# Kernel optimization log

Hardware: AMD Instinct MI355X
Metric: run time of the kernel (lower is better)

## Reference

```python
import math
import jax, jax.numpy as jnp
import numpy as np

B, S, D, H = 4, 2048, 1024, 16
HD = D // H
SAMPLING_FACTOR = 5.0


def setup_inputs() -> dict:
    key = jax.random.key(0)
    ks = jax.random.split(key, 6)
    std = 1.0 / math.sqrt(D)
    inp = {
        "x": jax.random.normal(ks[0], (B, S, D), dtype=jnp.float32),
        "Wq": jax.random.normal(ks[1], (D, D), dtype=jnp.float32) * std,
        "bq": jnp.zeros((D,), dtype=jnp.float32),
        "Wk": jax.random.normal(ks[2], (D, D), dtype=jnp.float32) * std,
        "bk": jnp.zeros((D,), dtype=jnp.float32),
        "Wv": jax.random.normal(ks[3], (D, D), dtype=jnp.float32) * std,
        "bv": jnp.zeros((D,), dtype=jnp.float32),
        "Wo": jax.random.normal(ks[4], (D, D), dtype=jnp.float32) * std,
        "bo": jnp.zeros((D,), dtype=jnp.float32),
        "sample_idx": jax.random.randint(ks[5], (S,), 0, S, dtype=jnp.int32),
    }
    return inp


def reference(x, Wq, bq, Wk, bk, Wv, bv, Wo, bo, sample_idx):
    batch, seq_len, d_model = x.shape
    scale = math.sqrt(HD)
    # u = number of top (active) queries; U_part = seq_len here (sampling saturates)
    u = max(1, min(seq_len, int(SAMPLING_FACTOR * math.log(seq_len + 1))))

    def proj(W, b):
        # [B,S,D] -> [B,H,S,hd]
        return (x @ W + b).reshape(batch, seq_len, H, HD).transpose(0, 2, 1, 3)

    Q = proj(Wq, bq)
    K = proj(Wk, bk)
    V = proj(Wv, bv)

    # sparsity measure over sampled keys (with replacement)
    K_sample = K[:, :, sample_idx, :]                     # [B,H,U,hd]
    scores_sample = jnp.einsum("bhsd,bhud->bhsu", Q, K_sample) / scale
    M = scores_sample.max(axis=-1) - scores_sample.mean(axis=-1)  # [B,H,S]

    _, top_idx = jax.lax.top_k(M, u)                      # [B,H,u]

    Q_reduce = jnp.take_along_axis(Q, top_idx[..., None], axis=2)  # [B,H,u,hd]
    attn_scores = jnp.einsum("bhud,bhsd->bhus", Q_reduce, K) / scale
    attn_probs = jax.nn.softmax(attn_scores, axis=-1)
    context = jnp.einsum("bhus,bhsd->bhud", attn_probs, V)        # [B,H,u,hd]

    # fill lazy queries with mean of V, scatter active-query contexts
    V_mean = V.mean(axis=2, keepdims=True)                # [B,H,1,hd]
    out = jnp.broadcast_to(V_mean, (batch, H, seq_len, HD))
    b_idx = jnp.arange(batch)[:, None, None]
    h_idx = jnp.arange(H)[None, :, None]
    out = out.at[b_idx, h_idx, top_idx].set(context)      # [B,H,S,hd]

    out = out.transpose(0, 2, 1, 3).reshape(batch, seq_len, d_model)
    return out @ Wo + bo
```

## Files before the change

### kernel.cpp

```cpp
#include <hip/hip_runtime.h>
#include <math.h>
#include <stdint.h>
#include <stddef.h>

#define BB 4
#define SS 2048
#define DD 1024
#define HH 16
#define HD 64
#define UU 38
#define BH (BB*HH)
#define NROWS (BB*SS)
#define QSZ (BB*HH*SS*HD)
#define NSPLIT 8
#define SPLEN (SS/NSPLIT)
#define QPAD 40

typedef unsigned short ushortT;
typedef unsigned int u32;
typedef __attribute__((ext_vector_type(8))) short bf16x8;
typedef __attribute__((ext_vector_type(4))) float f32x4;

static __device__ __forceinline__ ushortT f2bf(float f) {
  union { float f; unsigned int u; } v; v.f = f;
  unsigned int r = v.u + 0x7fffu + ((v.u >> 16) & 1u);
  return (ushortT)(r >> 16);
}
static __device__ __forceinline__ float bf2f(ushortT h) {
  union { unsigned int u; float f; } v; v.u = ((unsigned int)h) << 16; return v.f;
}
static __device__ __forceinline__ void gld16(const void* g, void* l) {
  __builtin_amdgcn_global_load_lds((const __attribute__((address_space(1))) u32*)g,
                                   (__attribute__((address_space(3))) u32*)l, 16, 0, 0);
}

__global__ __launch_bounds__(256) void split_x(
    const float* __restrict__ x, ushortT* __restrict__ xh, ushortT* __restrict__ xl)
{
  size_t i = ((size_t)blockIdx.x * 256 + threadIdx.x) * 8;
  float4 v0 = *(const float4*)&x[i];
  float4 v1 = *(const float4*)&x[i + 4];
  float fv[8] = {v0.x, v0.y, v0.z, v0.w, v1.x, v1.y, v1.z, v1.w};
  bf16x8 hv, lv;
#pragma unroll
  for (int j = 0; j < 8; ++j) {
    ushortT h = f2bf(fv[j]);
    hv[j] = (short)h;
    lv[j] = (short)f2bf(fv[j] - bf2f(h));
  }
  *(bf16x8*)&xh[i] = hv;
  *(bf16x8*)&xl[i] = lv;
}

__global__ __launch_bounds__(256) void splitT_kernel(
    const float* __restrict__ W, ushortT* __restrict__ WhT, ushortT* __restrict__ WlT)
{
  __shared__ float tile[64][65];
  const int t = threadIdx.x;
  const int bk = blockIdx.y * 64, bn = blockIdx.x * 64;
  const int rr = t >> 4, c4 = (t & 15) * 4;
#pragma unroll
  for (int p = 0; p < 4; ++p) {
    int row = rr + p * 16;
    float4 v = *(const float4*)&W[(size_t)(bk + row) * DD + bn + c4];
    tile[row][c4] = v.x; tile[row][c4+1] = v.y; tile[row][c4+2] = v.z; tile[row][c4+3] = v.w;
  }
  __syncthreads();
  const int n = t & 63, ks = (t >> 6) * 16;
  union { ushortT us[16]; uint4 q[2]; } hb, lb;
#pragma unroll
  for (int j = 0; j < 16; ++j) {
    float f = tile[ks + j][n];
    ushortT h = f2bf(f);
    hb.us[j] = h;
    lb.us[j] = f2bf(f - bf2f(h));
  }
  size_t o = ((size_t)(bn + n) * DD + (size_t)(bk + ks)) >> 3;
  ((uint4*)WhT)[o] = hb.q[0]; ((uint4*)WhT)[o + 1] = hb.q[1];
  ((uint4*)WlT)[o] = lb.q[0]; ((uint4*)WlT)[o + 1] = lb.q[1];
}

__global__ __launch_bounds__(256) void dedupe_kernel(
    const int* __restrict__ sidx, int* __restrict__ uidx, int* __restrict__ ucount)
{
  __shared__ unsigned bm[64];
  __shared__ int base[64];
  const int t = threadIdx.x;
  if (t < 64) bm[t] = 0;
  __syncthreads();
  for (int s = t; s < SS; s += 256) {
    int v = sidx[s];
    atomicOr(&bm[v >> 5], 1u << (v & 31));
  }
  __syncthreads();
  if (t < 64) {
    int c = __popc(bm[t]);
    int pre = c;
#pragma unroll
    for (int off = 1; off < 64; off <<= 1) {
      int o = __shfl_up(pre, off, 64);
      if (t >= off) pre += o;
    }
    base[t] = pre - c;
    if (t == 63) ucount[0] = pre;
  }
  __syncthreads();
  if (t < 64) {
    unsigned m = bm[t];
    int o = base[t];
    while (m) {
      int b = __ffs(m) - 1;
      uidx[o++] = t * 32 + b;
      m &= m - 1;
    }
  }
  __syncthreads();
  int total = ucount[0];
  int padded = (total + 127) & ~127;
  int first = uidx[0];
  for (int i = total + t; i < padded; i += 256) uidx[i] = first;
}

__global__ __launch_bounds__(256, 4) void gemm_qkv(
    const ushortT* __restrict__ Axh, const ushortT* __restrict__ Axl,
    const ushortT* __restrict__ WqhT, const ushortT* __restrict__ WqlT,
    const ushortT* __restrict__ WkhT, const ushortT* __restrict__ WklT,
    const ushortT* __restrict__ WvhT, const ushortT* __restrict__ WvlT,
    const float* __restrict__ bq, const float* __restrict__ bk, const float* __restrict__ bv,
    ushortT* __restrict__ Qhg, ushortT* __restrict__ Qlg,
    ushortT* __restrict__ Khg, ushortT* __restrict__ Klg,
    float* __restrict__ V)
{
  __shared__ ushortT As[128 * 64];
  __shared__ ushortT Bs[128 * 64];
  const int t = threadIdx.x;
  const int lin = blockIdx.x;
  const int xcd = lin & 7;
  const int idx = lin >> 3;
  const int m_loc = idx & 7;
  const int n_idx = idx >> 3;
  const int m0 = (xcd * 8 + m_loc) * 128;
  const int p = n_idx >> 3;
  const int n0 = (n_idx & 7) * 128;
  const ushortT* Bh = (p == 0) ? WqhT : (p == 1) ? WkhT : WvhT;
  const ushortT* Bl = (p == 0) ? WqlT : (p == 1) ? WklT : WvlT;
  const float* bias = (p == 0) ? bq : (p == 1) ? bk : bv;
  const int lane = t & 63, w = t >> 6;
  const int wr = w >> 1, wc = w & 1;
  const int fr = lane & 15, fs = lane >> 4;
  const int srow = t >> 3, sslot = t & 7;
  f32x4 acc[4][4];
#pragma unroll
  for (int i = 0; i < 4; ++i)
#pragma unroll
    for (int j = 0; j < 4; ++j) acc[i][j] = (f32x4){0.f, 0.f, 0.f, 0.f};

  for (int kt = 0; kt < 48; ++kt) {
    const int seg = kt >> 4;
    const int rk0 = (kt & 15) * 64;
    const ushortT* a_src = (seg == 1) ? Axl : Axh;
    const ushortT* b_src = (seg == 2) ? Bl : Bh;
    __syncthreads();
#pragma unroll
    for (int is = 0; is < 4; ++is) {
      int row = is * 32 + srow;
      int soff = ((sslot ^ (row & 7)) * 8);
      int cb = (is * 256 + (t & 192)) * 8;
      gld16(&a_src[(size_t)(m0 + row) * DD + rk0 + soff], &As[cb]);
      gld16(&b_src[(size_t)(n0 + row) * DD + rk0 + soff], &Bs[cb]);
    }
    __syncthreads();
#pragma unroll
    for (int kk = 0; kk < 2; ++kk) {
      bf16x8 af[4], bf[4];
#pragma unroll
      for (int i = 0; i < 4; ++i) {
        int row = wr * 64 + i * 16 + fr;
        af[i] = *(const bf16x8*)&As[row * 64 + (((kk * 4 + fs) ^ (row & 7)) * 8)];
      }
#pragma unroll
      for (int j = 0; j < 4; ++j) {
        int row = wc * 64 + j * 16 + fr;
        bf[j] = *(const bf16x8*)&Bs[row * 64 + (((kk * 4 + fs) ^ (row & 7)) * 8)];
      }
#pragma unroll
      for (int i = 0; i < 4; ++i)
#pragma unroll
        for (int j = 0; j < 4; ++j)
          acc[i][j] = __builtin_amdgcn_mfma_f32_16x16x32_bf16(af[i], bf[j], acc[i][j], 0, 0, 0);
    }
  }
#pragma unroll
  for (int i = 0; i < 4; ++i) {
#pragma unroll
    for (int j = 0; j < 4; ++j) {
      int c = n0 + wc * 64 + j * 16 + fr;
      float bs = bias[c];
      int h = c >> 6, hd = c & 63;
#pragma unroll
      for (int r = 0; r < 4; ++r) {
        int m = m0 + wr * 64 + i * 16 + fs * 4 + r;
        int b = m >> 11, s = m & (SS - 1);
        size_t oidx = (((size_t)(b * HH + h)) * SS + s) * HD + hd;
        float val = acc[i][j][r] + bs;
        if (p == 2) {
          V[oidx] = val;
        } else {
          ushortT hv = f2bf(val);
          ushortT lv = f2bf(val - bf2f(hv));
          if (p == 0) { Qhg[oidx] = hv; Qlg[oidx] = lv; }
          else        { Khg[oidx] = hv; Klg[oidx] = lv; }
        }
      }
    }
  }
}

__global__ __launch_bounds__(256) void means_kernel(
    const ushortT* __restrict__ Khg, const ushortT* __restrict__ Klg,
    const float* __restrict__ V, const int* __restrict__ sidx,
    float* __restrict__ Kmean, float* __restrict__ Vmean)
{
  __shared__ float rk[4][64], rv[4][64];
  const int bh = blockIdx.x;
  const int t = threadIdx.x;
  const int d = t & 63, p = t >> 6;
  const float* Vb = V + (size_t)bh * SS * HD;
  float ka = 0.f, va = 0.f;
  for (int r = p * 512; r < (p + 1) * 512; ++r) {
    size_t ki = ((size_t)bh * SS + sidx[r]) * HD + d;
    ka += bf2f(Khg[ki]) + bf2f(Klg[ki]);
    va += Vb[(size_t)r * HD + d];
  }
  rk[p][d] = ka; rv[p][d] = va;
  __syncthreads();
  if (t < 64) {
    Kmean[bh * HD + t] = (rk[0][t] + rk[1][t] + rk[2][t] + rk[3][t]) * (1.0f / SS);
    Vmean[bh * HD + t] = (rv[0][t] + rv[1][t] + rv[2][t] + rv[3][t]) * (1.0f / SS);
  }
}

__global__ __launch_bounds__(256, 2) void m_mfma(
    const ushortT* __restrict__ Qhg, const ushortT* __restrict__ Qlg,
    const ushortT* __restrict__ Khg, const ushortT* __restrict__ Klg,
    const int* __restrict__ uidx, const int* __restrict__ ucount,
    const float* __restrict__ Kmean, float* __restrict__ M)
{
  __shared__ ushortT QhL[128 * 64], QlL[128 * 64], KhL[128 * 64], KlL[128 * 64];
  __shared__ float Mred[2][128];
  __shared__ float km[64];
  const int t = threadIdx.x;
  const int lin = blockIdx.x;
  const int swz = (lin & 7) * 128 + (lin >> 3);
  const int bh = swz >> 4;
  const int s0 = (swz & 15) * 128;
  const int lane = t & 63, w = t >> 6;
  const int wr = w >> 1, wc = w & 1;
  const int fr = lane & 15, fs = lane >> 4;
  if (t < 64) km[t] = Kmean[bh * HD + t];
  const int srow = t >> 3, sslot = t & 7;
  const int ntiles = (ucount[0] + 127) >> 7;
#pragma unroll
  for (int is = 0; is < 4; ++is) {
    int row = is * 32 + srow;
    int soff = ((sslot ^ (row & 7)) * 8);
    int cb = (is * 256 + (t & 192)) * 8;
    size_t ga = ((size_t)bh * SS + s0 + row) * HD + soff;
    gld16(&Qhg[ga], &QhL[cb]);
    gld16(&Qlg[ga], &QlL[cb]);
  }
  float runmax[4][4];
#pragma unroll
  for (int i = 0; i < 4; ++i)
#pragma unroll
    for (int r = 0; r < 4; ++r) runmax[i][r] = -INFINITY;

  for (int ui = 0; ui < ntiles; ++ui) {
    __syncthreads();
#pragma unroll
    for (int is = 0; is < 4; ++is) {
      int row = is * 32 + srow;
      int gr = uidx[ui * 128 + row];
      int soff = ((sslot ^ (row & 7)) * 8);
      int cb = (is * 256 + (t & 192)) * 8;
      size_t ga = ((size_t)bh * SS + gr) * HD + soff;
      gld16(&Khg[ga], &KhL[cb]);
      gld16(&Klg[ga], &KlL[cb]);
    }
    __syncthreads();
    f32x4 acc[4][4];
#pragma unroll
    for (int i = 0; i < 4; ++i)
#pragma unroll
      for (int j = 0; j < 4; ++j) acc[i][j] = (f32x4){0.f, 0.f, 0.f, 0.f};
#pragma unroll
    for (int kk = 0; kk < 2; ++kk) {
      bf16x8 ah[4], al[4], bh[4], bl[4];
#pragma unroll
      for (int i = 0; i < 4; ++i) {
        int row = wr * 64 + i * 16 + fr;
        int off = row * 64 + (((kk * 4 + fs) ^ (row & 7)) * 8);
        ah[i] = *(const bf16x8*)&QhL[off];
        al[i] = *(const bf16x8*)&QlL[off];
      }
#pragma unroll
      for (int j = 0; j < 4; ++j) {
        int row = wc * 64 + j * 16 + fr;
        int off = row * 64 + (((kk * 4 + fs) ^ (row & 7)) * 8);
        bh[j] = *(const bf16x8*)&KhL[off];
        bl[j] = *(const bf16x8*)&KlL[off];
      }
#pragma unroll
      for (int i = 0; i < 4; ++i)
#pragma unroll
        for (int j = 0; j < 4; ++j) {
          acc[i][j] = __builtin_amdgcn_mfma_f32_16x16x32_bf16(ah[i], bh[j], acc[i][j], 0, 0, 0);
          acc[i][j] = __builtin_amdgcn_mfma_f32_16x16x32_bf16(ah[i], bl[j], acc[i][j], 0, 0, 0);
          acc[i][j] = __builtin_amdgcn_mfma_f32_16x16x32_bf16(al[i], bh[j], acc[i][j], 0, 0, 0);
        }
    }
#pragma unroll
    for (int i = 0; i < 4; ++i)
#pragma unroll
      for (int j = 0; j < 4; ++j)
#pragma unroll
        for (int r = 0; r < 4; ++r) runmax[i][r] = fmaxf(runmax[i][r], acc[i][j][r]);
  }
#pragma unroll
  for (int i = 0; i < 4; ++i)
#pragma unroll
    for (int r = 0; r < 4; ++r) {
      float v = runmax[i][r];
      v = fmaxf(v, __shfl_xor(v, 1, 64));
      v = fmaxf(v, __shfl_xor(v, 2, 64));
      v = fmaxf(v, __shfl_xor(v, 4, 64));
      v = fmaxf(v, __shfl_xor(v, 8, 64));
      runmax[i][r] = v;
    }
  if (fr == 0) {
#pragma unroll
    for (int i = 0; i < 4; ++i)
#pragma unroll
      for (int r = 0; r < 4; ++r)
        Mred[wc][wr * 64 + i * 16 + fs * 4 + r] = runmax[i][r];
  }
  __syncthreads();
  if (t < 128) {
    float mx = fmaxf(Mred[0][t], Mred[1][t]);
    float md = 0.f;
    const ushortT* qh = &Qhg[((size_t)bh * SS + s0 + t) * HD];
    const ushortT* ql = &Qlg[((size_t)bh * SS + s0 + t) * HD];
#pragma unroll
    for (int k8 = 0; k8 < 8; ++k8) {
      bf16x8 hv = *(const bf16x8*)&qh[k8 * 8];
      bf16x8 lv = *(const bf16x8*)&ql[k8 * 8];
#pragma unroll
      for (int j = 0; j < 8; ++j)
        md += (bf2f((ushortT)hv[j]) + bf2f((ushortT)lv[j])) * km[k8 * 8 + j];
    }
    M[(size_t)bh * SS + s0 + t] = (mx - md) * 0.125f;
  }
}

__global__ __launch_bounds__(256) void topk_kernel(const float* __restrict__ M,
                                                   int* __restrict__ topi)
{
  __shared__ float rw[4];
  __shared__ int   ri4[4];
  __shared__ int   winner;
  const int t = threadIdx.x, bh = blockIdx.x;
  const int lane = t & 63, w = t >> 6;
  float v[8];
#pragma unroll
  for (int j = 0; j < 8; ++j) v[j] = M[(size_t)bh * SS + t + j * 256];
  for (int it = 0; it < UU; ++it) {
    float bv = v[0]; int bj = 0;
#pragma unroll
    for (int j = 1; j < 8; ++j) if (v[j] > bv) { bv = v[j]; bj = j; }
    int bs = t + bj * 256;
#pragma unroll
    for (int off = 32; off > 0; off >>= 1) {
      float ov = __shfl_xor(bv, off, 64);
      int os = __shfl_xor(bs, off, 64);
      if (ov > bv || (ov == bv && os < bs)) { bv = ov; bs = os; }
    }
    if (lane == 0) { rw[w] = bv; ri4[w] = bs; }
    __syncthreads();
    if (t == 0) {
      float fv = rw[0]; int fsx = ri4[0];
#pragma unroll
      for (int g = 1; g < 4; ++g)
        if (rw[g] > fv || (rw[g] == fv && ri4[g] < fsx)) { fv = rw[g]; fsx = ri4[g]; }
      topi[bh * UU + it] = fsx;
      winner = fsx;
    }
    __syncthreads();
    int wi = winner;
    if ((wi & 255) == t) {
      int jj = wi >> 8;
#pragma unroll
      for (int j = 0; j < 8; ++j) if (j == jj) v[j] = -INFINITY;
    }
  }
}

__global__ __launch_bounds__(256) void attn_flash(
    const ushortT* __restrict__ Qhg, const ushortT* __restrict__ Qlg,
    const ushortT* __restrict__ Khg, const ushortT* __restrict__ Klg,
    const float* __restrict__ V, const int* __restrict__ topi,
    float* __restrict__ pacc, float* __restrict__ pm, float* __restrict__ pl)
{
  __shared__ float Qt[64][68];
  __shared__ float KV[64][68];
  __shared__ float Ps[64][68];
  __shared__ float redA[16][64];
  __shared__ float redB[16][64];
  __shared__ float mrow[64], lrow[64], scl[64];
  const int t  = threadIdx.x;
  const int bh = blockIdx.x;
  const int sp = blockIdx.y;
  const float* Vb = V + (size_t)bh * SS * HD;
  if (t < 64) { mrow[t] = -INFINITY; lrow[t] = 0.f; }
  {
    int q = t >> 2, k4 = (t & 3) * 16;
    float fv[16];
#pragma unroll
    for (int e = 0; e < 16; ++e) fv[e] = 0.f;
    if (q < UU) {
      int qidx = topi[bh * UU + q];
      size_t ga = ((size_t)bh * SS + qidx) * HD + k4;
      bf16x8 h0 = *(const bf16x8*)&Qhg[ga];
      bf16x8 h1 = *(const bf16x8*)&Qhg[ga + 8];
      bf16x8 l0 = *(const bf16x8*)&Qlg[ga];
      bf16x8 l1 = *(const bf16x8*)&Qlg[ga + 8];
#pragma unroll
      for (int j = 0; j < 8; ++j) {
        fv[j]     = bf2f((ushortT)h0[j]) + bf2f((ushortT)l0[j]);
        fv[8 + j] = bf2f((ushortT)h1[j]) + bf2f((ushortT)l1[j]);
      }
    }
#pragma unroll
    for (int e = 0; e < 16; ++e) Qt[k4 + e][q] = fv[e];
  }
  const int q4 = (t & 15) * 4, j4g = (t >> 4) * 4, d4 = (t >> 4) * 4;
  const int lj = t >> 2, lk4 = (t & 3) * 16;
  float acc[4][4] = {};
  for (int s0 = sp * SPLEN; s0 < (sp + 1) * SPLEN; s0 += 64) {
    __syncthreads();
    {
      size_t ga = ((size_t)bh * SS + s0 + lj) * HD + lk4;
      bf16x8 h0 = *(const bf16x8*)&Khg[ga];
      bf16x8 h1 = *(const bf16x8*)&Khg[ga + 8];
      bf16x8 l0 = *(const bf16x8*)&Klg[ga];
      bf16x8 l1 = *(const bf16x8*)&Klg[ga + 8];
#pragma unroll
      for (int j = 0; j < 8; ++j) {
        KV[lk4 + j][lj]     = bf2f((ushortT)h0[j]) + bf2f((ushortT)l0[j]);
        KV[lk4 + 8 + j][lj] = bf2f((ushortT)h1[j]) + bf2f((ushortT)l1[j]);
      }
    }
    __syncthreads();
    float sacc[4][4] = {};
#pragma unroll 16
    for (int k = 0; k < 64; ++k) {
      float4 a = *(const float4*)&Qt[k][q4];
      float4 b = *(const float4*)&KV[k][j4g];
      sacc[0][0] += a.x*b.x; sacc[0][1] += a.x*b.y; sacc[0][2] += a.x*b.z; sacc[0][3] += a.x*b.w;
      sacc[1][0] += a.y*b.x; sacc[1][1] += a.y*b.y; sacc[1][2] += a.y*b.z; sacc[1][3] += a.y*b.w;
      sacc[2][0] += a.z*b.x; sacc[2][1] += a.z*b.y; sacc[2][2] += a.z*b.z; sacc[2][3] += a.z*b.w;
      sacc[3][0] += a.w*b.x; sacc[3][1] += a.w*b.y; sacc[3][2] += a.w*b.z; sacc[3][3] += a.w*b.w;
    }
#pragma unroll
    for (int i = 0; i < 4; ++i) {
      float mx = fmaxf(fmaxf(sacc[i][0], sacc[i][1]), fmaxf(sacc[i][2], sacc[i][3]));
      redA[t >> 4][q4 + i] = mx;
    }
    __syncthreads();
    if (t < 64) {
      float mx = redA[0][t];
#pragma unroll
      for (int g = 1; g < 16; ++g) mx = fmaxf(mx, redA[g][t]);
      float mn = fmaxf(mrow[t], mx * 0.125f);
      scl[t] = __expf(mrow[t] - mn);
      mrow[t] = mn;
    }
    __syncthreads();
    float4 vld[4];
#pragma unroll
    for (int i = 0; i < 4; ++i)
      vld[i] = *(const float4*)&Vb[(size_t)(s0 + lj) * HD + lk4 + 4 * i];
    float psum[4] = {};
#pragma unroll
    for (int i = 0; i < 4; ++i) {
#pragma unroll
      for (int j = 0; j < 4; ++j) {
        float e = __expf(sacc[i][j] * 0.125f - mrow[q4 + i]);
        Ps[j4g + j][q4 + i] = e;
        psum[i] += e;
      }
      redB[t >> 4][q4 + i] = psum[i];
    }
#pragma unroll
    for (int i = 0; i < 4; ++i)
      *(float4*)&KV[lj][lk4 + 4 * i] = vld[i];
    __syncthreads();
    if (t < 64) {
      float ts = redB[0][t];
#pragma unroll
      for (int g = 1; g < 16; ++g) ts += redB[g][t];
      lrow[t] = lrow[t] * scl[t] + ts;
    }
#pragma unroll
    for (int i = 0; i < 4; ++i) {
      float fsc = scl[q4 + i];
      acc[i][0] *= fsc; acc[i][1] *= fsc; acc[i][2] *= fsc; acc[i][3] *= fsc;
    }
#pragma unroll 16
    for (int j = 0; j < 64; ++j) {
      float4 a = *(const float4*)&Ps[j][q4];
      float4 b = *(const float4*)&KV[j][d4];
      acc[0][0] += a.x*b.x; acc[0][1] += a.x*b.y; acc[0][2] += a.x*b.z; acc[0][3] += a.x*b.w;
      acc[1][0] += a.y*b.x; acc[1][1] += a.y*b.y; acc[1][2] += a.y*b.z; acc[1][3] += a.y*b.w;
      acc[2][0] += a.z*b.x; acc[2][1] += a.z*b.y; acc[2][2] += a.z*b.z; acc[2][3] += a.z*b.w;
      acc[3][0] += a.w*b.x; acc[3][1] += a.w*b.y; acc[3][2] += a.w*b.z; acc[3][3] += a.w*b.w;
    }
  }
  const size_t pb = ((size_t)bh * NSPLIT + sp) * QPAD;
#pragma unroll
  for (int i = 0; i < 4; ++i) {
    int q = q4 + i;
    if (q < UU) {
#pragma unroll
      for (int j = 0; j < 4; ++j)
        pacc[(pb + q) * HD + d4 + j] = acc[i][j];
    }
  }
  if (t < UU) { pm[pb + t] = mrow[t]; pl[pb + t] = lrow[t]; }
}

__global__ __launch_bounds__(256) void attn_combine(
    const float* __restrict__ pacc, const float* __restrict__ pm,
    const float* __restrict__ pl, float* __restrict__ ctx)
{
  const int t  = threadIdx.x;
  const int bh = blockIdx.x;
  const int d = t & 63, qg = t >> 6;
  for (int q = qg; q < UU; q += 4) {
    float mv[NSPLIT];
    float ms = -INFINITY;
#pragma unroll
    for (int sp = 0; sp < NSPLIT; ++sp) {
      mv[sp] = pm[((size_t)bh * NSPLIT + sp) * QPAD + q];
      ms = fmaxf(ms, mv[sp]);
    }
    float l = 0.f, c = 0.f;
#pragma unroll
    for (int sp = 0; sp < NSPLIT; ++sp) {
      float wv = __expf(mv[sp] - ms);
      l += wv * pl[((size_t)bh * NSPLIT + sp) * QPAD + q];
      c += wv * pacc[(((size_t)bh * NSPLIT + sp) * QPAD + q) * HD + d];
    }
    ctx[((size_t)bh * UU + q) * HD + d] = c / l;
  }
}

__global__ __launch_bounds__(256) void base_kernel(
    const float* __restrict__ Vmean, const float* __restrict__ Wo,
    const float* __restrict__ bo, float* __restrict__ base)
{
  __shared__ float red[16][BB][16];
  const int t = threadIdx.x;
  const int cl = t & 15, kg = t >> 4;
  const int c = blockIdx.x * 16 + cl;
  float acc[BB] = {};
  for (int k = kg * 64; k < kg * 64 + 64; ++k) {
    float w = Wo[(size_t)k * DD + c];
#pragma unroll
    for (int b = 0; b < BB; ++b) acc[b] += Vmean[b * DD + k] * w;
  }
#pragma unroll
  for (int b = 0; b < BB; ++b) red[kg][b][cl] = acc[b];
  __syncthreads();
  if (t < 64) {
    int b = t >> 4, cc = blockIdx.x * 16 + (t & 15);
    float s = 0.f;
#pragma unroll
    for (int g = 0; g < 16; ++g) s += red[g][b][t & 15];
    base[b * DD + cc] = s + bo[cc];
  }
}

__global__ void fill_kernel(const float* __restrict__ base, float* __restrict__ out)
{
  size_t i = (size_t)blockIdx.x * 256 + threadIdx.x;
  float4 bv = ((const float4*)base)[(i >> 19) * 256 + (i & 255)];
  ((float4*)out)[i] = bv;
}

__global__ __launch_bounds__(256) void scatter_kernel(
    const float* __restrict__ ctx, const float* __restrict__ Vmean,
    const int* __restrict__ topi, const float* __restrict__ Wo,
    float* __restrict__ out)
{
  __shared__ float delta[64];
  const int t  = threadIdx.x;
  const int bh = blockIdx.x;
  const int u  = blockIdx.y;
  const int b = bh >> 4, h = bh & 15;
  const int s = topi[bh * UU + u];
  if (t < 64) delta[t] = ctx[((size_t)bh * UU + u) * HD + t] - Vmean[bh * HD + t];
  __syncthreads();
  float* orow = out + ((size_t)b * SS + s) * DD;
#pragma unroll
  for (int j = 0; j < 4; ++j) {
    int c = t + j * 256;
    float acc = 0.f;
#pragma unroll 8
    for (int d = 0; d < 64; ++d) acc += delta[d] * Wo[(size_t)(h * HD + d) * DD + c];
    atomicAdd(&orow[c], acc);
  }
}

extern "C" void kernel_launch(void* const* d_in, const int* in_sizes, int n_in,
                              void* d_out, int out_size, void* d_ws, size_t ws_size,
                              hipStream_t stream) {
  const float* x  = (const float*)d_in[0];
  const float* Wq = (const float*)d_in[1];
  const float* bq = (const float*)d_in[2];
  const float* Wk = (const float*)d_in[3];
  const float* bk = (const float*)d_in[4];
  const float* Wv = (const float*)d_in[5];
  const float* bv = (const float*)d_in[6];
  const float* Wo = (const float*)d_in[7];
  const float* bo = (const float*)d_in[8];
  const int* sidx = (const int*)d_in[9];
  float* out = (float*)d_out;

  float* f     = (float*)d_ws;
  float* V     = f;
  float* Kmean = f + (size_t)QSZ;
  float* Vmean = Kmean + BH * HD;
  float* Mbuf  = Vmean + BH * HD;
  float* base  = Mbuf + (size_t)BH * SS;
  float* ctx   = base + BB * DD;
  float* pacc  = ctx + (size_t)BH * UU * HD;
  float* pm    = pacc + (size_t)BH * NSPLIT * QPAD * HD;
  float* pl    = pm + (size_t)BH * NSPLIT * QPAD;
  int*   topi  = (int*)(pl + (size_t)BH * NSPLIT * QPAD);
  int*   uidx  = topi + 4096;
  int*   ucount= uidx + 4096;
  ushortT* usp = (ushortT*)(ucount + 64);
  ushortT* WqhT = usp;
  ushortT* WqlT = WqhT + (size_t)DD * DD;
  ushortT* WkhT = WqlT + (size_t)DD * DD;
  ushortT* WklT = WkhT + (size_t)DD * DD;
  ushortT* WvhT = WklT + (size_t)DD * DD;
  ushortT* WvlT = WvhT + (size_t)DD * DD;
  ushortT* xh   = WvlT + (size_t)DD * DD;
  ushortT* xl   = xh + (size_t)NROWS * DD;
  ushortT* Qhg  = xl + (size_t)NROWS * DD;
  ushortT* Qlg  = Qhg + (size_t)QSZ;
  ushortT* Khg  = Qlg + (size_t)QSZ;
  ushortT* Klg  = Khg + (size_t)QSZ;

  split_x<<<NROWS * DD / (256 * 8), 256, 0, stream>>>(x, xh, xl);
  dim3 gs(16, 16);
  splitT_kernel<<<gs, 256, 0, stream>>>(Wq, WqhT, WqlT);
  splitT_kernel<<<gs, 256, 0, stream>>>(Wk, WkhT, WklT);
  splitT_kernel<<<gs, 256, 0, stream>>>(Wv, WvhT, WvlT);
  dedupe_kernel<<<1, 256, 0, stream>>>(sidx, uidx, ucount);
  gemm_qkv<<<1536, 256, 0, stream>>>(xh, xl, WqhT, WqlT, WkhT, WklT, WvhT, WvlT,
                                     bq, bk, bv, Qhg, Qlg, Khg, Klg, V);
  means_kernel<<<BH, 256, 0, stream>>>(Khg, Klg, V, sidx, Kmean, Vmean);
  m_mfma<<<1024, 256, 0, stream>>>(Qhg, Qlg, Khg, Klg, uidx, ucount, Kmean, Mbuf);
  topk_kernel<<<BH, 256, 0, stream>>>(Mbuf, topi);
  attn_flash<<<dim3(BH, NSPLIT), 256, 0, stream>>>(Qhg, Qlg, Khg, Klg, V, topi, pacc, pm, pl);
  attn_combine<<<BH, 256, 0, stream>>>(pacc, pm, pl, ctx);
  base_kernel<<<DD / 16, 256, 0, stream>>>(Vmean, Wo, bo, base);
  fill_kernel<<<(NROWS * DD / 4) / 256, 256, 0, stream>>>(base, out);
  scatter_kernel<<<dim3(BH, UU), 256, 0, stream>>>(ctx, Vmean, topi, Wo, out);
}
```

Measured before the change: 430.6 us.

## Read Q fragments from global in m_mfma, retile QKV grid, double split count

```diff
diff --git a/kernel.cpp b/kernel.cpp
--- a/kernel.cpp
+++ b/kernel.cpp
@@ -12,7 +12,7 @@
 #define BH (BB*HH)
 #define NROWS (BB*SS)
 #define QSZ (BB*HH*SS*HD)
-#define NSPLIT 8
+#define NSPLIT 16
 #define SPLEN (SS/NSPLIT)
 #define QPAD 40
 
@@ -137,8 +137,11 @@
   const int lin = blockIdx.x;
   const int xcd = lin & 7;
   const int idx = lin >> 3;
-  const int m_loc = idx & 7;
-  const int n_idx = idx >> 3;
+  const int msub = idx & 3;
+  const int rest = idx >> 2;
+  const int n_idx = rest % 24;
+  const int half = rest / 24;
+  const int m_loc = half * 4 + msub;
   const int m0 = (xcd * 8 + m_loc) * 128;
   const int p = n_idx >> 3;
   const int n0 = (n_idx & 7) * 128;
@@ -240,13 +243,13 @@
   }
 }
 
-__global__ __launch_bounds__(256, 2) void m_mfma(
+__global__ __launch_bounds__(256, 3) void m_mfma(
     const ushortT* __restrict__ Qhg, const ushortT* __restrict__ Qlg,
     const ushortT* __restrict__ Khg, const ushortT* __restrict__ Klg,
     const int* __restrict__ uidx, const int* __restrict__ ucount,
     const float* __restrict__ Kmean, float* __restrict__ M)
 {
-  __shared__ ushortT QhL[128 * 64], QlL[128 * 64], KhL[128 * 64], KlL[128 * 64];
+  __shared__ ushortT KhL[128 * 64], KlL[128 * 64];
   __shared__ float Mred[2][128];
   __shared__ float km[64];
   const int t = threadIdx.x;
@@ -260,15 +263,7 @@
   if (t < 64) km[t] = Kmean[bh * HD + t];
   const int srow = t >> 3, sslot = t & 7;
   const int ntiles = (ucount[0] + 127) >> 7;
-#pragma unroll
-  for (int is = 0; is < 4; ++is) {
-    int row = is * 32 + srow;
-    int soff = ((sslot ^ (row & 7)) * 8);
-    int cb = (is * 256 + (t & 192)) * 8;
-    size_t ga = ((size_t)bh * SS + s0 + row) * HD + soff;
-    gld16(&Qhg[ga], &QhL[cb]);
-    gld16(&Qlg[ga], &QlL[cb]);
-  }
+  const size_t qbase = (size_t)bh * SS + s0;
   float runmax[4][4];
 #pragma unroll
   for (int i = 0; i < 4; ++i)
@@ -298,10 +293,9 @@
       bf16x8 ah[4], al[4], bh[4], bl[4];
 #pragma unroll
       for (int i = 0; i < 4; ++i) {
-        int row = wr * 64 + i * 16 + fr;
-        int off = row * 64 + (((kk * 4 + fs) ^ (row & 7)) * 8);
-        ah[i] = *(const bf16x8*)&QhL[off];
-        al[i] = *(const bf16x8*)&QlL[off];
+        size_t ga = (qbase + (size_t)(wr * 64 + i * 16 + fr)) * HD + kk * 32 + fs * 8;
+        ah[i] = *(const bf16x8*)&Qhg[ga];
+        al[i] = *(const bf16x8*)&Qlg[ga];
       }
 #pragma unroll
       for (int j = 0; j < 4; ++j) {
@@ -348,8 +342,8 @@
   if (t < 128) {
     float mx = fmaxf(Mred[0][t], Mred[1][t]);
     float md = 0.f;
-    const ushortT* qh = &Qhg[((size_t)bh * SS + s0 + t) * HD];
-    const ushortT* ql = &Qlg[((size_t)bh * SS + s0 + t) * HD];
+    const ushortT* qh = &Qhg[(qbase + t) * HD];
+    const ushortT* ql = &Qlg[(qbase + t) * HD];
 #pragma unroll
     for (int k8 = 0; k8 < 8; ++k8) {
       bf16x8 hv = *(const bf16x8*)&qh[k8 * 8];
```

Result: no change. 438.1 us (+1.7%).
